# Optimization experiments

Measured on AMD Instinct MI355X. Metric: run time of the kernel, lower is better.

The kernel has to match this reference:

```python
import jax, jax.numpy as jnp
import numpy as np

N = 50000      # total atoms in batched graph
E = 800000     # edges
IN = 128       # in_feats
OUT = 64       # out_feats (per GAT head)
H = 4          # num_heads
NEG_SLOPE = 0.2
BN_EPS = 1e-5


def setup_inputs() -> dict:
    key = jax.random.key(0)
    ks = jax.random.split(key, 16)
    s = 0.1  # keep activations well-scaled
    return {
        "node_feats": jax.random.normal(ks[0], (N, IN), jnp.float32),
        "W_fc":       jax.random.normal(ks[1], (IN, H * OUT), jnp.float32) * s,
        "attn_l":     jax.random.normal(ks[2], (H, OUT), jnp.float32) * s,
        "attn_r":     jax.random.normal(ks[3], (H, OUT), jnp.float32) * s,
        "gat_res_w":  jax.random.normal(ks[4], (IN, H * OUT), jnp.float32) * s,
        "gat_bias":   jax.random.normal(ks[5], (H * OUT,), jnp.float32) * s,
        "conv_w":     jax.random.normal(ks[6], (1, H, 1), jnp.float32) * s,
        "conv_b":     jax.random.normal(ks[7], (1,), jnp.float32) * s,
        "res_w":      jax.random.normal(ks[8], (IN, OUT), jnp.float32) * s,
        "res_b":      jax.random.normal(ks[9], (OUT,), jnp.float32) * s,
        "bn_gamma":   jnp.ones((OUT,), jnp.float32),
        "bn_beta":    jnp.zeros((OUT,), jnp.float32),
        "src":        jax.random.randint(ks[10], (E,), 0, N, jnp.int32),
        "dst":        jax.random.randint(ks[11], (E,), 0, N, jnp.int32),
        "etype":      0,
    }


def reference(node_feats, W_fc, attn_l, attn_r, gat_res_w, gat_bias,
              conv_w, conv_b, res_w, res_b, bn_gamma, bn_beta,
              src, dst, etype):
    # ---- GATConv (DGL semantics, eval mode: no dropout) ----
    h = (node_feats @ W_fc).reshape(-1, H, OUT)            # [N,H,D]
    el = jnp.sum(h * attn_l, axis=-1)                      # [N,H]
    er = jnp.sum(h * attn_r, axis=-1)                      # [N,H]
    e = jax.nn.leaky_relu(el[src] + er[dst], NEG_SLOPE)    # [E,H]
    # segment softmax over incoming edges of each dst node
    m = jax.ops.segment_max(e, dst, num_segments=N)        # [N,H]
    m = jnp.where(jnp.isfinite(m), m, 0.0)                 # empty segments
    a = jnp.exp(e - m[dst])                                # [E,H]
    ssum = jax.ops.segment_sum(a, dst, num_segments=N)     # [N,H]
    alpha = a / (ssum[dst] + 1e-16)                        # [E,H]
    # weighted aggregation: rst[v] = sum_{(u->v)} alpha * h[u]
    rst = jax.ops.segment_sum(alpha[:, :, None] * h[src], dst, num_segments=N)  # [N,H,D]
    # GAT residual (in != H*OUT -> linear res_fc, no bias) + bias + activation
    rst = rst + (node_feats @ gat_res_w).reshape(-1, H, OUT) + gat_bias.reshape(H, OUT)
    rst = jax.nn.relu(rst)                                 # [N,H,D]
    # ---- Conv1d(4 -> 1, kernel=1): weighted head merge ----
    y = jnp.einsum("nhd,h->nd", rst, conv_w[0, :, 0]) + conv_b[0]  # [N,D]
    # ---- outer residual ----
    y = y + jax.nn.relu(node_feats @ res_w + res_b)
    # ---- BatchNorm1d (training-style batch stats) ----
    mean = jnp.mean(y, axis=0)
    var = jnp.var(y, axis=0)
    return (y - mean) / jnp.sqrt(var + BN_EPS) * bn_gamma + bn_beta
```

## Files before the change

kernel.cpp:

```cpp
#include <hip/hip_runtime.h>

#define IN_F   128
#define OUTD   64
#define HOUT   256
#define NEG_SLOPE 0.2f
#define BN_EPS 1e-5f
#define HISTB  512

typedef __attribute__((ext_vector_type(8))) short bf16x8;
typedef __attribute__((ext_vector_type(4))) float f32x4;
typedef __attribute__((ext_vector_type(2))) float f32x2;

__device__ __forceinline__ unsigned short f2bf(float f) {
    union { float f; unsigned u; } v; v.f = f;
    unsigned r = (v.u + 0x7FFF + ((v.u >> 16) & 1)) >> 16;
    return (unsigned short)r;
}
__device__ __forceinline__ float bf2f(unsigned short h) {
    union { unsigned u; float f; } v; v.u = ((unsigned)h) << 16;
    return v.f;
}

__device__ __forceinline__ int b2idx(int c, int k) {
    int tt, j;
    if (c < 256)      { tt = (c >> 4) & 3;                     j = c >> 6; }
    else if (c < 512) { int cc = c - 256; tt = 4 + ((cc >> 4) & 3); j = cc >> 6; }
    else if (c < 576) { int cc = c - 512; tt = 8;              j = cc >> 4; }
    else              { tt = 9;                                j = 0; }
    int n15 = c & 15;
    int ks = k >> 5, qd = (k >> 3) & 3, kk = k & 7;
    return ((((tt * 4 + j) * 4 + ks) * 64) + qd * 16 + n15) * 8 + kk;
}

__global__ __launch_bounds__(256) void k0_pack(
    const float* __restrict__ W_fc, const float* __restrict__ W_gres,
    const float* __restrict__ W_res,
    const float* __restrict__ attn_l, const float* __restrict__ attn_r,
    unsigned short* __restrict__ Btg2)
{
    int bid = blockIdx.x, t = threadIdx.x;
    if (bid < 288) {
        int idx = bid * 256 + t;
        int c = idx >> 7, k = idx & 127;
        float v;
        if (c < 256)      v = W_fc[k * HOUT + c];
        else if (c < 512) v = W_gres[k * HOUT + (c - 256)];
        else              v = W_res[k * OUTD + (c - 512)];
        Btg2[b2idx(c, k)] = f2bf(v);
        return;
    }
    for (int p = t; p < 512; p += 256) {
        int h = p >> 7, k = p & 127;
        float sl = 0.f, sr = 0.f;
        for (int d = 0; d < 64; ++d) {
            float wv = W_fc[k * HOUT + h * 64 + d];
            sl += wv * attn_l[h * 64 + d];
            sr += wv * attn_r[h * 64 + d];
        }
        Btg2[b2idx(576 + h, k)] = f2bf(sl);
        Btg2[b2idx(580 + h, k)] = f2bf(sr);
    }
    for (int p = t; p < 8 * 128; p += 256) {
        int c = 584 + (p >> 7), k = p & 127;
        Btg2[b2idx(c, k)] = 0;
    }
}

__global__ __launch_bounds__(256) void k1_gemm(
    const float* __restrict__ A, const unsigned short* __restrict__ Btg2,
    const float* __restrict__ gat_bias, const float* __restrict__ res_b,
    const int* __restrict__ dst, int* __restrict__ degree, int* __restrict__ rank,
    unsigned char* __restrict__ Hh8, unsigned char* __restrict__ Hr8,
    unsigned short* __restrict__ Rres,
    float* __restrict__ el, float* __restrict__ er,
    int N, int E)
{
    int t = threadIdx.x;

    if (blockIdx.x < HISTB) {
        int ht = blockIdx.x * 256 + t;
        for (int e = ht; e < E; e += HISTB * 256)
            rank[e] = atomicAdd(degree + dst[e], 1);
        return;
    }

    int w = t >> 6, lane = t & 63, quad = lane >> 4, n15 = lane & 15;
    int gw = (blockIdx.x - HISTB) * 4 + w;
    int T = (N + 15) / 16;
    if (gw >= T) return;

    int m0 = gw * 16;
    bool full = (m0 + 16 <= N);
    int lofs = (quad * 16 + n15) * 8;

    bf16x8 af[4];
    {
        int r = m0 + n15;
#pragma unroll
        for (int ks = 0; ks < 4; ++ks) {
            float4 v0 = make_float4(0.f, 0.f, 0.f, 0.f), v1 = v0;
            if (r < N) {
                const float* ap = A + (size_t)r * IN_F + ks * 32 + quad * 8;
                v0 = *(const float4*)ap;
                v1 = *(const float4*)(ap + 4);
            }
            bf16x8 o;
            o[0] = f2bf(v0.x); o[1] = f2bf(v0.y); o[2] = f2bf(v0.z); o[3] = f2bf(v0.w);
            o[4] = f2bf(v1.x); o[5] = f2bf(v1.y); o[6] = f2bf(v1.z); o[7] = f2bf(v1.w);
            af[ks] = o;
        }
    }

#pragma unroll
    for (int s = 0; s < 4; ++s) {
        f32x4 acc[4] = {};
#pragma unroll
        for (int ks = 0; ks < 4; ++ks) {
            bf16x8 bfr[4];
#pragma unroll
            for (int j = 0; j < 4; ++j)
                bfr[j] = *(const bf16x8*)(Btg2 + ((s * 16 + j * 4 + ks) << 9) + lofs);
#pragma unroll
            for (int j = 0; j < 4; ++j)
                acc[j] = __builtin_amdgcn_mfma_f32_16x16x32_bf16(af[ks], bfr[j], acc[j], 0, 0, 0);
        }
#pragma unroll
        for (int reg = 0; reg < 4; ++reg) {
            int r = m0 + quad * 4 + reg;
            if (full || r < N) {
                unsigned pk = (unsigned)__builtin_amdgcn_cvt_pk_fp8_f32(acc[0][reg], acc[1][reg], 0, false);
                pk = (unsigned)__builtin_amdgcn_cvt_pk_fp8_f32(acc[2][reg], acc[3][reg], (int)pk, true);
                *(unsigned*)(Hh8 + ((size_t)r << 8) + (s * 16 + n15) * 4) = pk;
            }
        }
    }

#pragma unroll
    for (int s = 0; s < 4; ++s) {
        f32x4 acc[4] = {};
#pragma unroll
        for (int ks = 0; ks < 4; ++ks) {
            bf16x8 bfr[4];
#pragma unroll
            for (int j = 0; j < 4; ++j)
                bfr[j] = *(const bf16x8*)(Btg2 + (((4 + s) * 16 + j * 4 + ks) << 9) + lofs);
#pragma unroll
            for (int j = 0; j < 4; ++j)
                acc[j] = __builtin_amdgcn_mfma_f32_16x16x32_bf16(af[ks], bfr[j], acc[j], 0, 0, 0);
        }
        float b0 = gat_bias[0 * 64 + s * 16 + n15];
        float b1 = gat_bias[1 * 64 + s * 16 + n15];
        float b2 = gat_bias[2 * 64 + s * 16 + n15];
        float b3 = gat_bias[3 * 64 + s * 16 + n15];
#pragma unroll
        for (int reg = 0; reg < 4; ++reg) {
            int r = m0 + quad * 4 + reg;
            if (full || r < N) {
                unsigned pk = (unsigned)__builtin_amdgcn_cvt_pk_fp8_f32(acc[0][reg] + b0, acc[1][reg] + b1, 0, false);
                pk = (unsigned)__builtin_amdgcn_cvt_pk_fp8_f32(acc[2][reg] + b2, acc[3][reg] + b3, (int)pk, true);
                *(unsigned*)(Hr8 + ((size_t)r << 8) + (s * 16 + n15) * 4) = pk;
            }
        }
    }

    {
        f32x4 acc[4] = {};
#pragma unroll
        for (int ks = 0; ks < 4; ++ks) {
            bf16x8 bfr[4];
#pragma unroll
            for (int j = 0; j < 4; ++j)
                bfr[j] = *(const bf16x8*)(Btg2 + ((8 * 16 + j * 4 + ks) << 9) + lofs);
#pragma unroll
            for (int j = 0; j < 4; ++j)
                acc[j] = __builtin_amdgcn_mfma_f32_16x16x32_bf16(af[ks], bfr[j], acc[j], 0, 0, 0);
        }
#pragma unroll
        for (int reg = 0; reg < 4; ++reg) {
            int r = m0 + quad * 4 + reg;
            if (full || r < N) {
#pragma unroll
                for (int j = 0; j < 4; ++j)
                    Rres[(size_t)r * OUTD + j * 16 + n15] = f2bf(acc[j][reg] + res_b[j * 16 + n15]);
            }
        }
    }

    {
        f32x4 acc2 = {};
#pragma unroll
        for (int ks = 0; ks < 4; ++ks) {
            bf16x8 b = *(const bf16x8*)(Btg2 + ((9 * 16 + ks) << 9) + lofs);
            acc2 = __builtin_amdgcn_mfma_f32_16x16x32_bf16(af[ks], b, acc2, 0, 0, 0);
        }
#pragma unroll
        for (int reg = 0; reg < 4; ++reg) {
            int r = m0 + quad * 4 + reg;
            if ((full || r < N) && n15 < 8) {
                float v = acc2[reg];
                if (n15 < 4) el[(size_t)r * 4 + n15] = v;
                else         er[(size_t)r * 4 + (n15 - 4)] = v;
            }
        }
    }
}

__global__ __launch_bounds__(256) void scanA_kernel(const int* __restrict__ degree,
                                                    int* __restrict__ excl,
                                                    int* __restrict__ blocksum, int N) {
    __shared__ int sm[256];
    int t = threadIdx.x;
    int i = blockIdx.x * 256 + t;
    int d = (i < N) ? degree[i] : 0;
    sm[t] = d; __syncthreads();
    for (int off = 1; off < 256; off <<= 1) {
        int v = (t >= off) ? sm[t - off] : 0;
        __syncthreads();
        sm[t] += v;
        __syncthreads();
    }
    if (i < N) excl[i] = sm[t] - d;
    if (t == 255) blocksum[blockIdx.x] = sm[255];
}

__global__ __launch_bounds__(256) void scanB_kernel(const int* __restrict__ blocksum,
                                                    int* __restrict__ base, int nb) {
    __shared__ int sm[256];
    int t = threadIdx.x;
    int d = (t < nb) ? blocksum[t] : 0;
    sm[t] = d; __syncthreads();
    for (int off = 1; off < 256; off <<= 1) {
        int v = (t >= off) ? sm[t - off] : 0;
        __syncthreads();
        sm[t] += v;
        __syncthreads();
    }
    if (t < nb) base[t] = sm[t] - d;
}

__global__ void scatter_kernel(const int* __restrict__ src, const int* __restrict__ dst,
                               const int* __restrict__ rank, const int* __restrict__ excl,
                               const int* __restrict__ base,
                               unsigned* __restrict__ usrc_sorted, int E) {
    int e = blockIdx.x * 256 + threadIdx.x;
    if (e >= E) return;
    int d = dst[e];
    int p = excl[d] + base[d >> 8] + rank[e];
    usrc_sorted[p] = (unsigned)src[e] << 8;
}

__global__ __launch_bounds__(256) void agg_kernel(
    const unsigned char* __restrict__ Hh8, const unsigned char* __restrict__ Hr8,
    const unsigned short* __restrict__ Rres, const float* __restrict__ el,
    const float* __restrict__ er,
    const int* __restrict__ excl, const int* __restrict__ base,
    const unsigned* __restrict__ usrc_sorted,
    const float* __restrict__ conv_w, const float* __restrict__ conv_b,
    float* __restrict__ y, int N, int E)
{
    int wave = threadIdx.x >> 6, lane = threadIdx.x & 63;
    int v = blockIdx.x * 4 + wave;
    if (v >= N) return;
    int b  = excl[v] + base[v >> 8];
    int e2 = (v + 1 < N) ? (excl[v + 1] + base[(v + 1) >> 8]) : E;
    int deg = e2 - b;

    float4 rv = *(const float4*)(er + (size_t)v * 4);
    const unsigned char* hbase = Hh8 + lane * 4;
    float a0 = 0.f, a1 = 0.f, a2 = 0.f, a3 = 0.f;
    float p0 = 0.f, p1 = 0.f, p2 = 0.f, p3 = 0.f;

    for (int i0 = 0; i0 < deg; i0 += 64) {
        int j = i0 + lane;
        unsigned ux = 0, s01 = 0, s23 = 0;
        if (j < deg) {
            ux = usrc_sorted[b + j];
            float4 l = *(const float4*)(el + ((size_t)(ux >> 8)) * 4);
            float x, s0, s1, s2, s3;
            x = l.x + rv.x; x = x > 0.f ? x : NEG_SLOPE * x; s0 = __expf(x);
            x = l.y + rv.y; x = x > 0.f ? x : NEG_SLOPE * x; s1 = __expf(x);
            x = l.z + rv.z; x = x > 0.f ? x : NEG_SLOPE * x; s2 = __expf(x);
            x = l.w + rv.w; x = x > 0.f ? x : NEG_SLOPE * x; s3 = __expf(x);
            p0 += s0; p1 += s1; p2 += s2; p3 += s3;
            s01 = (unsigned)f2bf(s0) | ((unsigned)f2bf(s1) << 16);
            s23 = (unsigned)f2bf(s2) | ((unsigned)f2bf(s3) << 16);
        }
        int cl = deg - i0; if (cl > 64) cl = 64;
        int jj = 0;
        for (; jj + 1 < cl; jj += 2) {
            unsigned uA   = (unsigned)__builtin_amdgcn_readlane((int)ux, jj);
            unsigned sA01 = (unsigned)__builtin_amdgcn_readlane((int)s01, jj);
            unsigned sA23 = (unsigned)__builtin_amdgcn_readlane((int)s23, jj);
            unsigned uB   = (unsigned)__builtin_amdgcn_readlane((int)ux, jj + 1);
            unsigned sB01 = (unsigned)__builtin_amdgcn_readlane((int)s01, jj + 1);
            unsigned sB23 = (unsigned)__builtin_amdgcn_readlane((int)s23, jj + 1);
            unsigned hvA = *(const unsigned*)(hbase + uA);
            unsigned hvB = *(const unsigned*)(hbase + uB);
            f32x2 loA = __builtin_amdgcn_cvt_pk_f32_fp8(hvA, false);
            f32x2 hiA = __builtin_amdgcn_cvt_pk_f32_fp8(hvA, true);
            f32x2 loB = __builtin_amdgcn_cvt_pk_f32_fp8(hvB, false);
            f32x2 hiB = __builtin_amdgcn_cvt_pk_f32_fp8(hvB, true);
            a0 += bf2f((unsigned short)(sA01 & 0xffff)) * loA.x;
            a1 += bf2f((unsigned short)(sA01 >> 16))    * loA.y;
            a2 += bf2f((unsigned short)(sA23 & 0xffff)) * hiA.x;
            a3 += bf2f((unsigned short)(sA23 >> 16))    * hiA.y;
            a0 += bf2f((unsigned short)(sB01 & 0xffff)) * loB.x;
            a1 += bf2f((unsigned short)(sB01 >> 16))    * loB.y;
            a2 += bf2f((unsigned short)(sB23 & 0xffff)) * hiB.x;
            a3 += bf2f((unsigned short)(sB23 >> 16))    * hiB.y;
        }
        if (jj < cl) {
            unsigned uA   = (unsigned)__builtin_amdgcn_readlane((int)ux, jj);
            unsigned sA01 = (unsigned)__builtin_amdgcn_readlane((int)s01, jj);
            unsigned sA23 = (unsigned)__builtin_amdgcn_readlane((int)s23, jj);
            unsigned hvA = *(const unsigned*)(hbase + uA);
            f32x2 loA = __builtin_amdgcn_cvt_pk_f32_fp8(hvA, false);
            f32x2 hiA = __builtin_amdgcn_cvt_pk_f32_fp8(hvA, true);
            a0 += bf2f((unsigned short)(sA01 & 0xffff)) * loA.x;
            a1 += bf2f((unsigned short)(sA01 >> 16))    * loA.y;
            a2 += bf2f((unsigned short)(sA23 & 0xffff)) * hiA.x;
            a3 += bf2f((unsigned short)(sA23 >> 16))    * hiA.y;
        }
    }
#pragma unroll
    for (int off = 1; off < 64; off <<= 1) {
        p0 += __shfl_xor(p0, off); p1 += __shfl_xor(p1, off);
        p2 += __shfl_xor(p2, off); p3 += __shfl_xor(p3, off);
    }
    float r0 = 1.f / (p0 + 1e-16f), r1 = 1.f / (p1 + 1e-16f);
    float r2 = 1.f / (p2 + 1e-16f), r3 = 1.f / (p3 + 1e-16f);

    unsigned hr = *(const unsigned*)(Hr8 + ((size_t)v << 8) + lane * 4);
    f32x2 rlo = __builtin_amdgcn_cvt_pk_f32_fp8(hr, false);
    f32x2 rhi = __builtin_amdgcn_cvt_pk_f32_fp8(hr, true);
    float resv = bf2f(Rres[(size_t)v * OUTD + lane]);
    float yv = conv_b[0] + (resv > 0.f ? resv : 0.f);
    float tt;
    tt = a0 * r0 + rlo.x; tt = tt > 0.f ? tt : 0.f; yv += conv_w[0] * tt;
    tt = a1 * r1 + rlo.y; tt = tt > 0.f ? tt : 0.f; yv += conv_w[1] * tt;
    tt = a2 * r2 + rhi.x; tt = tt > 0.f ? tt : 0.f; yv += conv_w[2] * tt;
    tt = a3 * r3 + rhi.y; tt = tt > 0.f ? tt : 0.f; yv += conv_w[3] * tt;
    y[(size_t)v * OUTD + lane] = yv;
}

__global__ __launch_bounds__(256) void bn_partial_kernel(const float* __restrict__ y,
                                                         float* __restrict__ bnsum,
                                                         float* __restrict__ bnsumsq, int total) {
    __shared__ float smem[256];
    int t = threadIdx.x;
    size_t idx = (size_t)blockIdx.x * 256 + t;
    size_t stride = (size_t)gridDim.x * 256;
    float sum = 0.f, sq = 0.f;
    for (; idx < (size_t)total; idx += stride) {
        float v = y[idx];
        sum += v; sq += v * v;
    }
    int d = t & 63;
    smem[t] = sum; __syncthreads();
    if (t < 64) atomicAdd(bnsum + d, smem[t] + smem[t + 64] + smem[t + 128] + smem[t + 192]);
    __syncthreads();
    smem[t] = sq; __syncthreads();
    if (t < 64) atomicAdd(bnsumsq + d, smem[t] + smem[t + 64] + smem[t + 128] + smem[t + 192]);
}

__global__ void norm_kernel(const float* __restrict__ y,
                            const float* __restrict__ bnsum, const float* __restrict__ bnsumsq,
                            const float* __restrict__ gamma, const float* __restrict__ beta,
                            float* __restrict__ out, int total4, float invN) {
    int idx = blockIdx.x * blockDim.x + threadIdx.x;
    if (idx >= total4) return;
    float4 v = *(const float4*)(y + (size_t)idx * 4);
    int d = (idx * 4) & 63;
    float4 o;
#pragma unroll
    for (int k = 0; k < 4; ++k) {
        float mean = bnsum[d + k] * invN;
        float var = bnsumsq[d + k] * invN - mean * mean;
        float sc = gamma[d + k] * rsqrtf(var + BN_EPS);
        float sh = beta[d + k] - mean * sc;
        (&o.x)[k] = (&v.x)[k] * sc + sh;
    }
    *(float4*)(out + (size_t)idx * 4) = o;
}

extern "C" void kernel_launch(void* const* d_in, const int* in_sizes, int n_in,
                              void* d_out, int out_size, void* d_ws, size_t ws_size,
                              hipStream_t stream) {
    const float* node_feats = (const float*)d_in[0];
    const float* W_fc       = (const float*)d_in[1];
    const float* attn_l     = (const float*)d_in[2];
    const float* attn_r     = (const float*)d_in[3];
    const float* gat_res_w  = (const float*)d_in[4];
    const float* gat_bias   = (const float*)d_in[5];
    const float* conv_w     = (const float*)d_in[6];
    const float* conv_b     = (const float*)d_in[7];
    const float* res_w      = (const float*)d_in[8];
    const float* res_b      = (const float*)d_in[9];
    const float* bn_gamma   = (const float*)d_in[10];
    const float* bn_beta    = (const float*)d_in[11];
    const int*   src        = (const int*)d_in[12];
    const int*   dst        = (const int*)d_in[13];

    const int N = in_sizes[0] / IN_F;
    const int E = in_sizes[12];
    const int nb = (N + 255) / 256;
    const int T = (N + 15) / 16;
    const int Gblocks = (T + 3) / 4;

    char* ws = (char*)d_ws;
    size_t off = 0;
    auto alloc = [&](size_t bytes) -> void* {
        void* p = (void*)(ws + off);
        off += (bytes + 255) & ~(size_t)255;
        return p;
    };

    int*   degree  = (int*)alloc((size_t)N * 4);
    float* bnsum   = (float*)alloc(64 * 4);
    float* bnsumsq = (float*)alloc(64 * 4);
    size_t zero_bytes = off;
    int*            rank        = (int*)alloc((size_t)E * 4);
    int*            excl        = (int*)alloc((size_t)N * 4);
    int*            blocksum    = (int*)alloc(256 * 4);
    int*            base        = (int*)alloc(256 * 4);
    unsigned*       usrc_sorted = (unsigned*)alloc((size_t)E * 4);
    unsigned short* Btg2        = (unsigned short*)alloc((size_t)10 * 16 * 512 * 2);
    unsigned char*  Hh8         = (unsigned char*)alloc((size_t)N * 256);
    unsigned char*  Hr8         = (unsigned char*)alloc((size_t)N * 256);
    unsigned short* Rres        = (unsigned short*)alloc((size_t)N * OUTD * 2);
    float*          el          = (float*)alloc((size_t)N * 4 * 4);
    float*          er          = (float*)alloc((size_t)N * 4 * 4);
    float*          y           = (float*)alloc((size_t)N * OUTD * 4);
    (void)ws_size; (void)n_in; (void)out_size;

    hipMemsetAsync(d_ws, 0, zero_bytes, stream);

    k0_pack<<<289, 256, 0, stream>>>(W_fc, gat_res_w, res_w, attn_l, attn_r, Btg2);
    k1_gemm<<<HISTB + Gblocks, 256, 0, stream>>>(node_feats, Btg2, gat_bias, res_b,
                                                 dst, degree, rank, Hh8, Hr8, Rres,
                                                 el, er, N, E);
    scanA_kernel<<<nb, 256, 0, stream>>>(degree, excl, blocksum, N);
    scanB_kernel<<<1, 256, 0, stream>>>(blocksum, base, nb);
    scatter_kernel<<<(E + 255) / 256, 256, 0, stream>>>(src, dst, rank, excl, base,
                                                        usrc_sorted, E);
    agg_kernel<<<(N + 3) / 4, 256, 0, stream>>>(Hh8, Hr8, Rres, el, er, excl, base,
                                                usrc_sorted, conv_w, conv_b, y, N, E);
    bn_partial_kernel<<<512, 256, 0, stream>>>(y, bnsum, bnsumsq, N * OUTD);
    norm_kernel<<<(N * OUTD / 4 + 255) / 256, 256, 0, stream>>>(y, bnsum, bnsumsq,
                                                                bn_gamma, bn_beta, (float*)d_out,
                                                                N * OUTD / 4, 1.f / (float)N);
}
```

Before: 249.7 us.

## Fuse block-sum scan into scatter and BN partial sums into aggregation

Each scatter block now redoes the small block-sum prefix scan in LDS, which removes the separate single-block scanB launch. The aggregation kernel also accumulates the BatchNorm sums and sums of squares through atomics into 8 replicated slots, which removes the extra pass over y. The norm kernel computes scale and shift once per block into shared memory, and the histogram blocks move after the GEMM blocks with the histogram block count halved. A single-block scan is still reused to fill base for agg, and the float atomics spread over 8 slots add contention in exchange for dropping a full read of y.

```diff
diff --git a/kernel.cpp b/kernel.cpp
--- a/kernel.cpp
+++ b/kernel.cpp
@@ -5,7 +5,7 @@
 #define HOUT   256
 #define NEG_SLOPE 0.2f
 #define BN_EPS 1e-5f
-#define HISTB  512
+#define HISTB  256
 
 typedef __attribute__((ext_vector_type(8))) short bf16x8;
 typedef __attribute__((ext_vector_type(4))) float f32x4;
@@ -73,19 +73,19 @@
     unsigned char* __restrict__ Hh8, unsigned char* __restrict__ Hr8,
     unsigned short* __restrict__ Rres,
     float* __restrict__ el, float* __restrict__ er,
-    int N, int E)
+    int N, int E, int Gblocks)
 {
     int t = threadIdx.x;
 
-    if (blockIdx.x < HISTB) {
-        int ht = blockIdx.x * 256 + t;
+    if (blockIdx.x >= Gblocks) {
+        int ht = (blockIdx.x - Gblocks) * 256 + t;
         for (int e = ht; e < E; e += HISTB * 256)
             rank[e] = atomicAdd(degree + dst[e], 1);
         return;
     }
 
     int w = t >> 6, lane = t & 63, quad = lane >> 4, n15 = lane & 15;
-    int gw = (blockIdx.x - HISTB) * 4 + w;
+    int gw = blockIdx.x * 4 + w;
     int T = (N + 15) / 16;
     if (gw >= T) return;
 
@@ -223,29 +223,29 @@
     if (t == 255) blocksum[blockIdx.x] = sm[255];
 }
 
-__global__ __launch_bounds__(256) void scanB_kernel(const int* __restrict__ blocksum,
-                                                    int* __restrict__ base, int nb) {
+__global__ __launch_bounds__(256) void scatter_kernel(
+    const int* __restrict__ src, const int* __restrict__ dst,
+    const int* __restrict__ rank, const int* __restrict__ excl,
+    const int* __restrict__ blocksum,
+    unsigned* __restrict__ usrc_sorted, int E, int nb) {
     __shared__ int sm[256];
+    __shared__ int base_lds[256];
     int t = threadIdx.x;
-    int d = (t < nb) ? blocksum[t] : 0;
-    sm[t] = d; __syncthreads();
+    int d0 = (t < nb) ? blocksum[t] : 0;
+    sm[t] = d0; __syncthreads();
     for (int off = 1; off < 256; off <<= 1) {
         int v = (t >= off) ? sm[t - off] : 0;
         __syncthreads();
         sm[t] += v;
         __syncthreads();
     }
-    if (t < nb) base[t] = sm[t] - d;
-}
-
-__global__ void scatter_kernel(const int* __restrict__ src, const int* __restrict__ dst,
-                               const int* __restrict__ rank, const int* __restrict__ excl,
-                               const int* __restrict__ base,
-                               unsigned* __restrict__ usrc_sorted, int E) {
-    int e = blockIdx.x * 256 + threadIdx.x;
+    base_lds[t] = sm[t] - d0;
+    __syncthreads();
+
+    int e = blockIdx.x * 256 + t;
     if (e >= E) return;
     int d = dst[e];
-    int p = excl[d] + base[d >> 8] + rank[e];
+    int p = excl[d] + base_lds[d >> 8] + rank[e];
     usrc_sorted[p] = (unsigned)src[e] << 8;
 }
 
@@ -256,130 +256,138 @@
     const int* __restrict__ excl, const int* __restrict__ base,
     const unsigned* __restrict__ usrc_sorted,
     const float* __restrict__ conv_w, const float* __restrict__ conv_b,
-    float* __restrict__ y, int N, int E)
+    float* __restrict__ y, float* __restrict__ bnsum8, float* __restrict__ bnsq8,
+    int N, int E)
 {
-    int wave = threadIdx.x >> 6, lane = threadIdx.x & 63;
+    __shared__ float smem[256];
+    __shared__ float smem2[256];
+    int t = threadIdx.x;
+    int wave = t >> 6, lane = t & 63;
     int v = blockIdx.x * 4 + wave;
-    if (v >= N) return;
-    int b  = excl[v] + base[v >> 8];
-    int e2 = (v + 1 < N) ? (excl[v + 1] + base[(v + 1) >> 8]) : E;
-    int deg = e2 - b;
-
-    float4 rv = *(const float4*)(er + (size_t)v * 4);
-    const unsigned char* hbase = Hh8 + lane * 4;
-    float a0 = 0.f, a1 = 0.f, a2 = 0.f, a3 = 0.f;
-    float p0 = 0.f, p1 = 0.f, p2 = 0.f, p3 = 0.f;
-
-    for (int i0 = 0; i0 < deg; i0 += 64) {
-        int j = i0 + lane;
-        unsigned ux = 0, s01 = 0, s23 = 0;
-        if (j < deg) {
-            ux = usrc_sorted[b + j];
-            float4 l = *(const float4*)(el + ((size_t)(ux >> 8)) * 4);
-            float x, s0, s1, s2, s3;
-            x = l.x + rv.x; x = x > 0.f ? x : NEG_SLOPE * x; s0 = __expf(x);
-            x = l.y + rv.y; x = x > 0.f ? x : NEG_SLOPE * x; s1 = __expf(x);
-            x = l.z + rv.z; x = x > 0.f ? x : NEG_SLOPE * x; s2 = __expf(x);
-            x = l.w + rv.w; x = x > 0.f ? x : NEG_SLOPE * x; s3 = __expf(x);
-            p0 += s0; p1 += s1; p2 += s2; p3 += s3;
-            s01 = (unsigned)f2bf(s0) | ((unsigned)f2bf(s1) << 16);
-            s23 = (unsigned)f2bf(s2) | ((unsigned)f2bf(s3) << 16);
-        }
-        int cl = deg - i0; if (cl > 64) cl = 64;
-        int jj = 0;
-        for (; jj + 1 < cl; jj += 2) {
-            unsigned uA   = (unsigned)__builtin_amdgcn_readlane((int)ux, jj);
-            unsigned sA01 = (unsigned)__builtin_amdgcn_readlane((int)s01, jj);
-            unsigned sA23 = (unsigned)__builtin_amdgcn_readlane((int)s23, jj);
-            unsigned uB   = (unsigned)__builtin_amdgcn_readlane((int)ux, jj + 1);
-            unsigned sB01 = (unsigned)__builtin_amdgcn_readlane((int)s01, jj + 1);
-            unsigned sB23 = (unsigned)__builtin_amdgcn_readlane((int)s23, jj + 1);
-            unsigned hvA = *(const unsigned*)(hbase + uA);
-            unsigned hvB = *(const unsigned*)(hbase + uB);
-            f32x2 loA = __builtin_amdgcn_cvt_pk_f32_fp8(hvA, false);
-            f32x2 hiA = __builtin_amdgcn_cvt_pk_f32_fp8(hvA, true);
-            f32x2 loB = __builtin_amdgcn_cvt_pk_f32_fp8(hvB, false);
-            f32x2 hiB = __builtin_amdgcn_cvt_pk_f32_fp8(hvB, true);
-            a0 += bf2f((unsigned short)(sA01 & 0xffff)) * loA.x;
-            a1 += bf2f((unsigned short)(sA01 >> 16))    * loA.y;
-            a2 += bf2f((unsigned short)(sA23 & 0xffff)) * hiA.x;
-            a3 += bf2f((unsigned short)(sA23 >> 16))    * hiA.y;
-            a0 += bf2f((unsigned short)(sB01 & 0xffff)) * loB.x;
-            a1 += bf2f((unsigned short)(sB01 >> 16))    * loB.y;
-            a2 += bf2f((unsigned short)(sB23 & 0xffff)) * hiB.x;
-            a3 += bf2f((unsigned short)(sB23 >> 16))    * hiB.y;
-        }
-        if (jj < cl) {
-            unsigned uA   = (unsigned)__builtin_amdgcn_readlane((int)ux, jj);
-            unsigned sA01 = (unsigned)__builtin_amdgcn_readlane((int)s01, jj);
-            unsigned sA23 = (unsigned)__builtin_amdgcn_readlane((int)s23, jj);
-            unsigned hvA = *(const unsigned*)(hbase + uA);
-            f32x2 loA = __builtin_amdgcn_cvt_pk_f32_fp8(hvA, false);
-            f32x2 hiA = __builtin_amdgcn_cvt_pk_f32_fp8(hvA, true);
-            a0 += bf2f((unsigned short)(sA01 & 0xffff)) * loA.x;
-            a1 += bf2f((unsigned short)(sA01 >> 16))    * loA.y;
-            a2 += bf2f((unsigned short)(sA23 & 0xffff)) * hiA.x;
-            a3 += bf2f((unsigned short)(sA23 >> 16))    * hiA.y;
-        }
-    }
-#pragma unroll
-    for (int off = 1; off < 64; off <<= 1) {
-        p0 += __shfl_xor(p0, off); p1 += __shfl_xor(p1, off);
-        p2 += __shfl_xor(p2, off); p3 += __shfl_xor(p3, off);
-    }
-    float r0 = 1.f / (p0 + 1e-16f), r1 = 1.f / (p1 + 1e-16f);
-    float r2 = 1.f / (p2 + 1e-16f), r3 = 1.f / (p3 + 1e-16f);
-
-    unsigned hr = *(const unsigned*)(Hr8 + ((size_t)v << 8) + lane * 4);
-    f32x2 rlo = __builtin_amdgcn_cvt_pk_f32_fp8(hr, false);
-    f32x2 rhi = __builtin_amdgcn_cvt_pk_f32_fp8(hr, true);
-    float resv = bf2f(Rres[(size_t)v * OUTD + lane]);
-    float yv = conv_b[0] + (resv > 0.f ? resv : 0.f);
-    float tt;
-    tt = a0 * r0 + rlo.x; tt = tt > 0.f ? tt : 0.f; yv += conv_w[0] * tt;
-    tt = a1 * r1 + rlo.y; tt = tt > 0.f ? tt : 0.f; yv += conv_w[1] * tt;
-    tt = a2 * r2 + rhi.x; tt = tt > 0.f ? tt : 0.f; yv += conv_w[2] * tt;
-    tt = a3 * r3 + rhi.y; tt = tt > 0.f ? tt : 0.f; yv += conv_w[3] * tt;
-    y[(size_t)v * OUTD + lane] = yv;
-}
-
-__global__ __launch_bounds__(256) void bn_partial_kernel(const float* __restrict__ y,
-                                                         float* __restrict__ bnsum,
-                                                         float* __restrict__ bnsumsq, int total) {
-    __shared__ float smem[256];
+
+    float yv = 0.f;
+    if (v < N) {
+        int b  = excl[v] + base[v >> 8];
+        int e2 = (v + 1 < N) ? (excl[v + 1] + base[(v + 1) >> 8]) : E;
+        int deg = e2 - b;
+
+        float4 rv = *(const float4*)(er + (size_t)v * 4);
+        const unsigned char* hbase = Hh8 + lane * 4;
+        float a0 = 0.f, a1 = 0.f, a2 = 0.f, a3 = 0.f;
+        float p0 = 0.f, p1 = 0.f, p2 = 0.f, p3 = 0.f;
+
+        for (int i0 = 0; i0 < deg; i0 += 64) {
+            int j = i0 + lane;
+            unsigned ux = 0, s01 = 0, s23 = 0;
+            if (j < deg) {
+                ux = usrc_sorted[b + j];
+                float4 l = *(const float4*)(el + ((size_t)(ux >> 8)) * 4);
+                float x, s0, s1, s2, s3;
+                x = l.x + rv.x; x = x > 0.f ? x : NEG_SLOPE * x; s0 = __expf(x);
+                x = l.y + rv.y; x = x > 0.f ? x : NEG_SLOPE * x; s1 = __expf(x);
+                x = l.z + rv.z; x = x > 0.f ? x : NEG_SLOPE * x; s2 = __expf(x);
+                x = l.w + rv.w; x = x > 0.f ? x : NEG_SLOPE * x; s3 = __expf(x);
+                p0 += s0; p1 += s1; p2 += s2; p3 += s3;
+                s01 = (unsigned)f2bf(s0) | ((unsigned)f2bf(s1) << 16);
+                s23 = (unsigned)f2bf(s2) | ((unsigned)f2bf(s3) << 16);
+            }
+            int cl = deg - i0; if (cl > 64) cl = 64;
+            int jj = 0;
+            for (; jj + 1 < cl; jj += 2) {
+                unsigned uA   = (unsigned)__builtin_amdgcn_readlane((int)ux, jj);
+                unsigned sA01 = (unsigned)__builtin_amdgcn_readlane((int)s01, jj);
+                unsigned sA23 = (unsigned)__builtin_amdgcn_readlane((int)s23, jj);
+                unsigned uB   = (unsigned)__builtin_amdgcn_readlane((int)ux, jj + 1);
+                unsigned sB01 = (unsigned)__builtin_amdgcn_readlane((int)s01, jj + 1);
+                unsigned sB23 = (unsigned)__builtin_amdgcn_readlane((int)s23, jj + 1);
+                unsigned hvA = *(const unsigned*)(hbase + uA);
+                unsigned hvB = *(const unsigned*)(hbase + uB);
+                f32x2 loA = __builtin_amdgcn_cvt_pk_f32_fp8(hvA, false);
+                f32x2 hiA = __builtin_amdgcn_cvt_pk_f32_fp8(hvA, true);
+                f32x2 loB = __builtin_amdgcn_cvt_pk_f32_fp8(hvB, false);
+                f32x2 hiB = __builtin_amdgcn_cvt_pk_f32_fp8(hvB, true);
+                a0 += bf2f((unsigned short)(sA01 & 0xffff)) * loA.x;
+                a1 += bf2f((unsigned short)(sA01 >> 16))    * loA.y;
+                a2 += bf2f((unsigned short)(sA23 & 0xffff)) * hiA.x;
+                a3 += bf2f((unsigned short)(sA23 >> 16))    * hiA.y;
+                a0 += bf2f((unsigned short)(sB01 & 0xffff)) * loB.x;
+                a1 += bf2f((unsigned short)(sB01 >> 16))    * loB.y;
+                a2 += bf2f((unsigned short)(sB23 & 0xffff)) * hiB.x;
+                a3 += bf2f((unsigned short)(sB23 >> 16))    * hiB.y;
+            }
+            if (jj < cl) {
+                unsigned uA   = (unsigned)__builtin_amdgcn_readlane((int)ux, jj);
+                unsigned sA01 = (unsigned)__builtin_amdgcn_readlane((int)s01, jj);
+                unsigned sA23 = (unsigned)__builtin_amdgcn_readlane((int)s23, jj);
+                unsigned hvA = *(const unsigned*)(hbase + uA);
+                f32x2 loA = __builtin_amdgcn_cvt_pk_f32_fp8(hvA, false);
+                f32x2 hiA = __builtin_amdgcn_cvt_pk_f32_fp8(hvA, true);
+                a0 += bf2f((unsigned short)(sA01 & 0xffff)) * loA.x;
+                a1 += bf2f((unsigned short)(sA01 >> 16))    * loA.y;
+                a2 += bf2f((unsigned short)(sA23 & 0xffff)) * hiA.x;
+                a3 += bf2f((unsigned short)(sA23 >> 16))    * hiA.y;
+            }
+        }
+#pragma unroll
+        for (int off = 1; off < 64; off <<= 1) {
+            p0 += __shfl_xor(p0, off); p1 += __shfl_xor(p1, off);
+            p2 += __shfl_xor(p2, off); p3 += __shfl_xor(p3, off);
+        }
+        float r0 = 1.f / (p0 + 1e-16f), r1 = 1.f / (p1 + 1e-16f);
+        float r2 = 1.f / (p2 + 1e-16f), r3 = 1.f / (p3 + 1e-16f);
+
+        unsigned hr = *(const unsigned*)(Hr8 + ((size_t)v << 8) + lane * 4);
+        f32x2 rlo = __builtin_amdgcn_cvt_pk_f32_fp8(hr, false);
+        f32x2 rhi = __builtin_amdgcn_cvt_pk_f32_fp8(hr, true);
+        float resv = bf2f(Rres[(size_t)v * OUTD + lane]);
+        yv = conv_b[0] + (resv > 0.f ? resv : 0.f);
+        float tt;
+        tt = a0 * r0 + rlo.x; tt = tt > 0.f ? tt : 0.f; yv += conv_w[0] * tt;
+        tt = a1 * r1 + rlo.y; tt = tt > 0.f ? tt : 0.f; yv += conv_w[1] * tt;
+        tt = a2 * r2 + rhi.x; tt = tt > 0.f ? tt : 0.f; yv += conv_w[2] * tt;
+        tt = a3 * r3 + rhi.y; tt = tt > 0.f ? tt : 0.f; yv += conv_w[3] * tt;
+        y[(size_t)v * OUTD + lane] = yv;
+    }
+
+    smem[t] = yv;
+    smem2[t] = yv * yv;
+    __syncthreads();
+    if (t < 64) {
+        float s = smem[t] + smem[t + 64] + smem[t + 128] + smem[t + 192];
+        float q = smem2[t] + smem2[t + 64] + smem2[t + 128] + smem2[t + 192];
+        int c = (blockIdx.x & 7) << 6;
+        atomicAdd(bnsum8 + c + t, s);
+        atomicAdd(bnsq8 + c + t, q);
+    }
+}
+
+__global__ __launch_bounds__(256) void norm_kernel(
+    const float* __restrict__ y,
+    const float* __restrict__ bnsum8, const float* __restrict__ bnsq8,
+    const float* __restrict__ gamma, const float* __restrict__ beta,
+    float* __restrict__ out, int total4, float invN) {
+    __shared__ float scale[64], shift[64];
     int t = threadIdx.x;
-    size_t idx = (size_t)blockIdx.x * 256 + t;
-    size_t stride = (size_t)gridDim.x * 256;
-    float sum = 0.f, sq = 0.f;
-    for (; idx < (size_t)total; idx += stride) {
-        float v = y[idx];
-        sum += v; sq += v * v;
-    }
-    int d = t & 63;
-    smem[t] = sum; __syncthreads();
-    if (t < 64) atomicAdd(bnsum + d, smem[t] + smem[t + 64] + smem[t + 128] + smem[t + 192]);
+    if (t < 64) {
+        float s = 0.f, q = 0.f;
+#pragma unroll
+        for (int c = 0; c < 8; ++c) { s += bnsum8[c * 64 + t]; q += bnsq8[c * 64 + t]; }
+        float mean = s * invN;
+        float var = q * invN - mean * mean;
+        float sc = gamma[t] * rsqrtf(var + BN_EPS);
+        scale[t] = sc;
+        shift[t] = beta[t] - mean * sc;
+    }
     __syncthreads();
-    smem[t] = sq; __syncthreads();
-    if (t < 64) atomicAdd(bnsumsq + d, smem[t] + smem[t + 64] + smem[t + 128] + smem[t + 192]);
-}
-
-__global__ void norm_kernel(const float* __restrict__ y,
-                            const float* __restrict__ bnsum, const float* __restrict__ bnsumsq,
-                            const float* __restrict__ gamma, const float* __restrict__ beta,
-                            float* __restrict__ out, int total4, float invN) {
-    int idx = blockIdx.x * blockDim.x + threadIdx.x;
+    int idx = blockIdx.x * blockDim.x + t;
     if (idx >= total4) return;
     float4 v = *(const float4*)(y + (size_t)idx * 4);
     int d = (idx * 4) & 63;
     float4 o;
-#pragma unroll
-    for (int k = 0; k < 4; ++k) {
-        float mean = bnsum[d + k] * invN;
-        float var = bnsumsq[d + k] * invN - mean * mean;
-        float sc = gamma[d + k] * rsqrtf(var + BN_EPS);
-        float sh = beta[d + k] - mean * sc;
-        (&o.x)[k] = (&v.x)[k] * sc + sh;
-    }
+    o.x = v.x * scale[d + 0] + shift[d + 0];
+    o.y = v.y * scale[d + 1] + shift[d + 1];
+    o.z = v.z * scale[d + 2] + shift[d + 2];
+    o.w = v.w * scale[d + 3] + shift[d + 3];
     *(float4*)(out + (size_t)idx * 4) = o;
 }
 
@@ -416,8 +424,8 @@
     };
 
     int*   degree  = (int*)alloc((size_t)N * 4);
-    float* bnsum   = (float*)alloc(64 * 4);
-    float* bnsumsq = (float*)alloc(64 * 4);
+    float* bnsum8  = (float*)alloc(8 * 64 * 4);
+    float* bnsq8   = (float*)alloc(8 * 64 * 4);
     size_t zero_bytes = off;
     int*            rank        = (int*)alloc((size_t)E * 4);
     int*            excl        = (int*)alloc((size_t)N * 4);
@@ -436,17 +444,19 @@
     hipMemsetAsync(d_ws, 0, zero_bytes, stream);
 
     k0_pack<<<289, 256, 0, stream>>>(W_fc, gat_res_w, res_w, attn_l, attn_r, Btg2);
-    k1_gemm<<<HISTB + Gblocks, 256, 0, stream>>>(node_feats, Btg2, gat_bias, res_b,
+    k1_gemm<<<Gblocks + HISTB, 256, 0, stream>>>(node_feats, Btg2, gat_bias, res_b,
                                                  dst, degree, rank, Hh8, Hr8, Rres,
-                                                 el, er, N, E);
+                                                 el, er, N, E, Gblocks);
     scanA_kernel<<<nb, 256, 0, stream>>>(degree, excl, blocksum, N);
-    scanB_kernel<<<1, 256, 0, stream>>>(blocksum, base, nb);
-    scatter_kernel<<<(E + 255) / 256, 256, 0, stream>>>(src, dst, rank, excl, base,
-                                                        usrc_sorted, E);
+    scatter_kernel<<<(E + 255) / 256, 256, 0, stream>>>(src, dst, rank, excl, blocksum,
+                                                        usrc_sorted, E, nb);
+    {
+        scanA_kernel<<<1, 256, 0, stream>>>(blocksum, base, (int*)(base + 256 - 1) , nb);
+    }
     agg_kernel<<<(N + 3) / 4, 256, 0, stream>>>(Hh8, Hr8, Rres, el, er, excl, base,
-                                                usrc_sorted, conv_w, conv_b, y, N, E);
-    bn_partial_kernel<<<512, 256, 0, stream>>>(y, bnsum, bnsumsq, N * OUTD);
-    norm_kernel<<<(N * OUTD / 4 + 255) / 256, 256, 0, stream>>>(y, bnsum, bnsumsq,
+                                                usrc_sorted, conv_w, conv_b, y,
+                                                bnsum8, bnsq8, N, E);
+    norm_kernel<<<(N * OUTD / 4 + 255) / 256, 256, 0, stream>>>(y, bnsum8, bnsq8,
                                                                 bn_gamma, bn_beta, (float*)d_out,
                                                                 N * OUTD / 4, 1.f / (float)N);
 }
```

After: 233.4 us. -6.5%, faster.
